# Optimization experiments

Measured on AMD Instinct MI355X. Metric: run time of the kernel, lower is better.

Reference implementation:

```python
import jax, jax.numpy as jnp
import numpy as np

NUM_HEADS = 16


def setup_inputs() -> dict:
    key = jax.random.key(0)
    ks = jax.random.split(key, 9)
    B, S, D = 2, 2048, 2048
    s = 1.0 / np.sqrt(D)
    return {
        "x": jax.random.normal(ks[0], (B, S, D), jnp.float32),
        "Wq": jax.random.normal(ks[1], (D, D), jnp.float32) * s,
        "bq": jax.random.normal(ks[2], (D,), jnp.float32) * 0.01,
        "Wk": jax.random.normal(ks[3], (D, D), jnp.float32) * s,
        "bk": jax.random.normal(ks[4], (D,), jnp.float32) * 0.01,
        "Wv": jax.random.normal(ks[5], (D, D), jnp.float32) * s,
        "bv": jax.random.normal(ks[6], (D,), jnp.float32) * 0.01,
        "Wo": jax.random.normal(ks[7], (D, D), jnp.float32) * s,
        "bo": jax.random.normal(ks[8], (D,), jnp.float32) * 0.01,
    }


def reference(x, Wq, bq, Wk, bk, Wv, bv, Wo, bo):
    B, S, D = x.shape
    H = NUM_HEADS
    dh = D // H
    # torch Linear: y = x @ W.T + b
    def proj(W, b):
        return (x @ W.T + b).reshape(B, S, H, dh).transpose(0, 2, 1, 3)  # [B,H,S,dh]
    Q = proj(Wq, bq)
    K = proj(Wk, bk)
    V = proj(Wv, bv)
    scores = jnp.einsum('bhqd,bhkd->bhqk', Q, K) / jnp.sqrt(jnp.float32(dh))
    causal = jnp.tril(jnp.ones((S, S), dtype=bool))  # allow k <= q
    scores = jnp.where(causal, scores, -jnp.inf)
    attn = jax.nn.softmax(scores, axis=-1)
    out = jnp.einsum('bhqk,bhkd->bhqd', attn, V)
    out = out.transpose(0, 2, 1, 3).reshape(B, S, D)
    return out @ Wo.T + bo
```

## Files before the change

### kernel.cpp

```cpp
#include <hip/hip_runtime.h>
#include <hip/hip_bf16.h>

#define B_  2
#define S_  2048
#define D_  2048
#define H_  16
#define DH_ 128
#define M_  (B_*S_)

typedef __hip_bfloat16 bf16;
typedef float v4f __attribute__((ext_vector_type(4)));
typedef short v8s __attribute__((ext_vector_type(8)));

__device__ __forceinline__ short f2s(float x) {
  bf16 h = __float2bfloat16(x);
  return *reinterpret_cast<const short*>(&h);
}
__device__ __forceinline__ v8s ld8(const float* p) {
  v4f a = *reinterpret_cast<const v4f*>(p);
  v4f b = *reinterpret_cast<const v4f*>(p + 4);
  v8s r = { f2s(a[0]), f2s(a[1]), f2s(a[2]), f2s(a[3]),
            f2s(b[0]), f2s(b[1]), f2s(b[2]), f2s(b[3]) };
  return r;
}
__device__ __forceinline__ void store_out(bf16* p, float v)  { *p = __float2bfloat16(v); }
__device__ __forceinline__ void store_out(float* p, float v) { *p = v; }

__device__ __forceinline__ void gll16(const bf16* g, bf16* l) {
  __builtin_amdgcn_global_load_lds((const __attribute__((address_space(1))) void*)g,
                                   (__attribute__((address_space(3))) void*)l,
                                   16, 0, 0);
}

__global__ __launch_bounds__(256) void cvt_f32_bf16(const float* __restrict__ in,
                                                    bf16* __restrict__ out, int n8) {
  int i = blockIdx.x * 256 + threadIdx.x;
  if (i >= n8) return;
  *reinterpret_cast<v8s*>(out + (size_t)i * 8) = ld8(in + (size_t)i * 8);
}

__global__ __launch_bounds__(256) void cvt3_f32_bf16(const float* __restrict__ a, bf16* __restrict__ oa,
                                                     const float* __restrict__ b, bf16* __restrict__ ob,
                                                     const float* __restrict__ c, bf16* __restrict__ oc) {
  const int bx = blockIdx.x;
  if (bx < 4096) {
    size_t i = (size_t)bx * 256 + threadIdx.x;
    *reinterpret_cast<v8s*>(oa + i * 8) = ld8(a + i * 8);
  } else if (bx < 6144) {
    size_t i = (size_t)(bx - 4096) * 256 + threadIdx.x;
    *reinterpret_cast<v8s*>(ob + i * 8) = ld8(b + i * 8);
  } else {
    size_t i = (size_t)(bx - 6144) * 256 + threadIdx.x;
    *reinterpret_cast<v8s*>(oc + i * 8) = ld8(c + i * 8);
  }
}

template <int MODE, typename TOUT>
__global__ __launch_bounds__(256) void gemm_bt(const bf16* __restrict__ A,
                                               const bf16* __restrict__ W,
                                               const float* __restrict__ bias0,
                                               const float* __restrict__ bias1,
                                               TOUT* __restrict__ out0,
                                               TOUT* __restrict__ out1) {
  __shared__ __align__(16) bf16 As[128 * 64];
  __shared__ __align__(16) bf16 Bs[128 * 64];
  const int tid  = threadIdx.x;
  const int lane = tid & 63, wave = tid >> 6;
  const int wm = wave >> 1, wn = wave & 1;
  const int quad = lane >> 4, l16 = lane & 15;
  const int swz  = l16 & 7;
  const int bm = blockIdx.y * 128, bn = blockIdx.x * 128;

  const bf16* Arow = A + (size_t)bm * D_;
  const bf16* Wrow = W + (size_t)bn * D_;

  v4f acc[4][4] = {};
  for (int k0 = 0; k0 < D_; k0 += 64) {
#pragma unroll
    for (int j = 0; j < 4; ++j) {
      const int blk = j * 256 + tid;
      const int row = blk >> 3, c = blk & 7;
      const int gcol = k0 + (((c ^ (row & 7)) << 3));
      gll16(Arow + (size_t)row * D_ + gcol, As + j * 2048 + wave * 512);
      gll16(Wrow + (size_t)row * D_ + gcol, Bs + j * 2048 + wave * 512);
    }
    __syncthreads();
    v8s af[4][2], bfr[4][2];
#pragma unroll
    for (int mi = 0; mi < 4; ++mi)
#pragma unroll
      for (int kk = 0; kk < 2; ++kk)
        af[mi][kk] = *reinterpret_cast<const v8s*>(
            &As[(wm * 64 + mi * 16 + l16) * 64 + (((kk * 4 + quad) ^ swz) << 3)]);
#pragma unroll
    for (int ni = 0; ni < 4; ++ni)
#pragma unroll
      for (int kk = 0; kk < 2; ++kk)
        bfr[ni][kk] = *reinterpret_cast<const v8s*>(
            &Bs[(wn * 64 + ni * 16 + l16) * 64 + (((kk * 4 + quad) ^ swz) << 3)]);
#pragma unroll
    for (int kk = 0; kk < 2; ++kk)
#pragma unroll
      for (int mi = 0; mi < 4; ++mi)
#pragma unroll
        for (int ni = 0; ni < 4; ++ni)
          acc[mi][ni] = __builtin_amdgcn_mfma_f32_16x16x32_bf16(
              af[mi][kk], bfr[ni][kk], acc[mi][ni], 0, 0, 0);
    __syncthreads();
  }

  constexpr float QSCALE = 0.12752003912f;
  const int proj = (MODE == 0) ? (bn >> 11) : 0;
  const float* bias = proj ? bias1 : bias0;
  TOUT* outp = proj ? out1 : out0;
  const int bnl = bn & 2047;
#pragma unroll
  for (int ni = 0; ni < 4; ++ni) {
    const int nl = bnl + wn * 64 + ni * 16 + l16;
    const float bv = bias[nl];
#pragma unroll
    for (int mi = 0; mi < 4; ++mi) {
      const int m0 = bm + wm * 64 + mi * 16 + quad * 4;
#pragma unroll
      for (int r = 0; r < 4; ++r) {
        const int m = m0 + r;
        float v = acc[mi][ni][r] + bv;
        size_t idx;
        if (MODE == 0) {
          if (!proj) v *= QSCALE;
          int b = m >> 11, s = m & (S_ - 1);
          int h = nl >> 7, d = nl & (DH_ - 1);
          idx = ((size_t)(b * H_ + h) * S_ + s) * DH_ + d;
        } else if (MODE == 2) {
          int b = m >> 11, s = m & (S_ - 1);
          int h = nl >> 7, d = nl & (DH_ - 1);
          idx = ((size_t)(b * H_ + h) * DH_ + d) * S_ + s;
        } else {
          idx = (size_t)m * D_ + nl;
        }
        store_out(outp + idx, v);
      }
    }
  }
}

#define QBLK 128
__global__ __launch_bounds__(512, 4) void attn_fused(const bf16* __restrict__ Q,
                                                     const bf16* __restrict__ K,
                                                     const bf16* __restrict__ Vt,
                                                     bf16* __restrict__ Oa) {
  __shared__ __align__(16) bf16 Ks[64 * 128];
  __shared__ __align__(16) bf16 Vs[128 * 64];
  __shared__ __align__(16) bf16 Ps[8][16 * 72];
  const int tid  = threadIdx.x;
  const int lane = tid & 63, wave = tid >> 6;
  const int quad = lane >> 4, l16 = lane & 15;
  const int swz  = l16 & 7;
  const int qtd = (int)gridDim.x - 1 - (int)blockIdx.x;
  const int qt  = (blockIdx.y & 16) ? (int)blockIdx.x : qtd;
  const int bh = blockIdx.y;
  const int b = bh >> 4, h = bh & 15;
  const bf16* Qh = Q  + (size_t)bh * S_ * DH_;
  const bf16* Kh = K  + (size_t)bh * S_ * DH_;
  const bf16* Vh = Vt + (size_t)bh * DH_ * S_;

  const int qrow0 = qt * QBLK + wave * 16;
  v8s qf[4];
#pragma unroll
  for (int kk = 0; kk < 4; ++kk)
    qf[kk] = *reinterpret_cast<const v8s*>(&Qh[(size_t)(qrow0 + l16) * DH_ + kk * 32 + quad * 8]);

  v4f acc_o[8] = {};
  float m_i[4], l_i[4];
#pragma unroll
  for (int r = 0; r < 4; ++r) { m_i[r] = -1.0e30f; l_i[r] = 0.f; }

  const int nkt = 2 * qt + 2;
  for (int kt = 0; kt < nkt; ++kt) {
    const int kbase = kt * 64;
#pragma unroll
    for (int rr = 0; rr < 2; ++rr) {
      const int g = rr * 512 + tid;
      const int krow = g >> 4, kc = g & 15;
      gll16(Kh + (size_t)(kbase + krow) * DH_ + ((kc ^ (krow & 7)) << 3),
            Ks + rr * 4096 + wave * 512);
      const int vrow = g >> 3, vc = g & 7;
      gll16(Vh + (size_t)vrow * S_ + kbase + ((vc ^ (vrow & 7)) << 3),
            Vs + rr * 4096 + wave * 512);
    }
    __syncthreads();

    const bool active = (kbase <= qrow0 + 15);
    if (active) {
      v4f sc[4];
      __builtin_amdgcn_s_setprio(1);
#pragma unroll
      for (int nt = 0; nt < 4; ++nt) {
        v4f a = {};
#pragma unroll
        for (int kk = 0; kk < 4; ++kk) {
          v8s kf = *reinterpret_cast<const v8s*>(
              &Ks[(nt * 16 + l16) * 128 + (((kk * 4 + quad) ^ swz) << 3)]);
          a = __builtin_amdgcn_mfma_f32_16x16x32_bf16(qf[kk], kf, a, 0, 0, 0);
        }
        sc[nt] = a;
      }
      __builtin_amdgcn_s_setprio(0);
      if (kbase + 63 > qrow0) {
#pragma unroll
        for (int nt = 0; nt < 4; ++nt)
#pragma unroll
          for (int r = 0; r < 4; ++r) {
            int kc2 = kbase + nt * 16 + l16;
            int qr = qrow0 + quad * 4 + r;
            if (kc2 > qr) sc[nt][r] = -1.0e30f;
          }
      }
#pragma unroll
      for (int r = 0; r < 4; ++r) {
        float mx = fmaxf(fmaxf(sc[0][r], sc[1][r]), fmaxf(sc[2][r], sc[3][r]));
        mx = fmaxf(mx, __shfl_xor(mx, 1));
        mx = fmaxf(mx, __shfl_xor(mx, 2));
        mx = fmaxf(mx, __shfl_xor(mx, 4));
        mx = fmaxf(mx, __shfl_xor(mx, 8));
        if (mx > m_i[r] + 8.0f) {
          float alpha = exp2f(m_i[r] - mx);
          m_i[r] = mx;
          l_i[r] *= alpha;
#pragma unroll
          for (int nt8 = 0; nt8 < 8; ++nt8) acc_o[nt8][r] *= alpha;
        }
        const float mm = m_i[r];
        float s0 = exp2f(sc[0][r] - mm);
        float s1 = exp2f(sc[1][r] - mm);
        float s2 = exp2f(sc[2][r] - mm);
        float s3 = exp2f(sc[3][r] - mm);
        sc[0][r] = s0; sc[1][r] = s1; sc[2][r] = s2; sc[3][r] = s3;
        float t = s0 + s1 + s2 + s3;
        t += __shfl_xor(t, 1); t += __shfl_xor(t, 2);
        t += __shfl_xor(t, 4); t += __shfl_xor(t, 8);
        l_i[r] += t;
      }
#pragma unroll
      for (int nt = 0; nt < 4; ++nt)
#pragma unroll
        for (int r = 0; r < 4; ++r)
          Ps[wave][(quad * 4 + r) * 72 + nt * 16 + l16] = __float2bfloat16(sc[nt][r]);
      asm volatile("s_waitcnt lgkmcnt(0)" ::: "memory");
      __builtin_amdgcn_s_setprio(1);
#pragma unroll
      for (int kk2 = 0; kk2 < 2; ++kk2) {
        v8s pf = *reinterpret_cast<const v8s*>(&Ps[wave][l16 * 72 + kk2 * 32 + quad * 8]);
#pragma unroll
        for (int nt8 = 0; nt8 < 8; ++nt8) {
          v8s vf = *reinterpret_cast<const v8s*>(
              &Vs[(nt8 * 16 + l16) * 64 + (((kk2 * 4 + quad) ^ swz) << 3)]);
          acc_o[nt8] = __builtin_amdgcn_mfma_f32_16x16x32_bf16(pf, vf, acc_o[nt8], 0, 0, 0);
        }
      }
      __builtin_amdgcn_s_setprio(0);
    }
    __syncthreads();
  }

#pragma unroll
  for (int r = 0; r < 4; ++r) {
    const float inv = 1.0f / l_i[r];
    const int srow = qrow0 + quad * 4 + r;
#pragma unroll
    for (int nt8 = 0; nt8 < 8; ++nt8)
      Oa[((size_t)b * S_ + srow) * D_ + h * DH_ + nt8 * 16 + l16] =
          __float2bfloat16(acc_o[nt8][r] * inv);
  }
}

extern "C" void kernel_launch(void* const* d_in, const int* in_sizes, int n_in,
                              void* d_out, int out_size, void* d_ws, size_t ws_size,
                              hipStream_t stream) {
  if (n_in != 9 ||
      in_sizes[0] != M_ * D_ ||
      in_sizes[1] != D_ * D_ || in_sizes[2] != D_ ||
      in_sizes[3] != D_ * D_ || in_sizes[4] != D_ ||
      in_sizes[5] != D_ * D_ || in_sizes[6] != D_ ||
      in_sizes[7] != D_ * D_ || in_sizes[8] != D_ ||
      out_size != M_ * D_)
    return;

  const float* x  = (const float*)d_in[0];
  const float* Wq = (const float*)d_in[1];
  const float* bq = (const float*)d_in[2];
  const float* Wk = (const float*)d_in[3];
  const float* bk = (const float*)d_in[4];
  const float* Wv = (const float*)d_in[5];
  const float* bv = (const float*)d_in[6];
  const float* Wo = (const float*)d_in[7];
  const float* bo = (const float*)d_in[8];
  float* out = (float*)d_out;

  const size_t NT = (size_t)M_ * D_;
  const size_t WN = (size_t)D_ * D_;
  bf16* qws   = (bf16*)d_out;
  bf16* xbf   = (bf16*)d_out + NT;
  bf16* kws   = (bf16*)d_ws;
  bf16* vtw   = kws + NT;
  bf16* aws   = vtw + NT;
  bf16* wqk   = aws;
  bf16* wv_s  = aws;
  bf16* wo_s  = kws;

  const int N8W = D_ * D_ / 8;

  dim3 bb(256);
  cvt3_f32_bf16<<<8192, bb, 0, stream>>>(x, xbf, Wq, wqk, Wk, wqk + WN);

  gemm_bt<0, bf16><<<dim3(32, 32), bb, 0, stream>>>(xbf, wqk, bq, bk, qws, kws);

  cvt_f32_bf16<<<N8W / 256, bb, 0, stream>>>(Wv, wv_s, N8W);
  gemm_bt<2, bf16><<<dim3(16, 32), bb, 0, stream>>>(xbf, wv_s, bv, bv, vtw, vtw);

  attn_fused<<<dim3(S_ / QBLK, B_ * H_), dim3(512), 0, stream>>>(qws, kws, vtw, aws);

  cvt_f32_bf16<<<N8W / 256, bb, 0, stream>>>(Wo, wo_s, N8W);
  gemm_bt<3, float><<<dim3(16, 32), bb, 0, stream>>>(aws, wo_s, bo, bo, out, out);
}
```

Baseline: 412.5 us.

## Add 256x256 double-buffered 8-wave GEMM for fused Q/K projection

Replaces the 128x128 single-buffered GEMM used for the combined Q/K projection with a 512-thread kernel that computes 256x256 tiles. Global-to-LDS loads for the next k-tile are issued in pieces interleaved with the MFMA phases, using ping-pong LDS buffers and explicit waitcnt/barriers. MFMA sections run at raised wave priority. The aim is more operand reuse per LDS load and hiding global load latency behind compute, at the cost of 128KB of LDS per block, fewer blocks (256), and fragile hand scheduling.

```diff
diff --git a/kernel.cpp b/kernel.cpp
--- a/kernel.cpp
+++ b/kernel.cpp
@@ -55,13 +55,156 @@
   }
 }
 
+template <int PR>
+__device__ __forceinline__ void stage_pair(const bf16* Arow, const bf16* Wrow,
+                                           int ktile, bf16* AsD, bf16* BsD,
+                                           int tid, int wave) {
+  const int k0 = ktile * 64;
+#pragma unroll
+  for (int u = 0; u < 2; ++u) {
+    const int i = PR * 2 + u;
+    const int blk = i * 512 + tid;
+    if (i < 4) {
+      const int row = blk >> 3, c = blk & 7;
+      gll16(Arow + (size_t)row * D_ + k0 + ((c ^ (row & 7)) << 3),
+            AsD + (i * 512 + wave * 64) * 8);
+    } else {
+      const int bb = blk - 2048;
+      const int row = bb >> 3, c = bb & 7;
+      gll16(Wrow + (size_t)row * D_ + k0 + ((c ^ (row & 7)) << 3),
+            BsD + ((i - 4) * 512 + wave * 64) * 8);
+    }
+  }
+}
+
+__global__ __launch_bounds__(512, 2) void gemm_qk8(const bf16* __restrict__ A,
+                                                   const bf16* __restrict__ W,
+                                                   const float* __restrict__ bias0,
+                                                   const float* __restrict__ bias1,
+                                                   bf16* __restrict__ out0,
+                                                   bf16* __restrict__ out1) {
+  __shared__ __align__(16) bf16 As0[256 * 64];
+  __shared__ __align__(16) bf16 Bs0[256 * 64];
+  __shared__ __align__(16) bf16 As1[256 * 64];
+  __shared__ __align__(16) bf16 Bs1[256 * 64];
+  const int tid  = threadIdx.x;
+  const int lane = tid & 63, wave = tid >> 6;
+  const int wm = wave >> 2, wn = wave & 3;
+  const int quad = lane >> 4, l16 = lane & 15;
+  const int swz  = l16 & 7;
+  const int bm = blockIdx.y * 256, bn = blockIdx.x * 256;
+  const bf16* Arow = A + (size_t)bm * D_;
+  const bf16* Wrow = W + (size_t)bn * D_;
+
+  v4f acc[8][4] = {};
+
+  stage_pair<0>(Arow, Wrow, 0, As0, Bs0, tid, wave);
+  stage_pair<1>(Arow, Wrow, 0, As0, Bs0, tid, wave);
+  stage_pair<2>(Arow, Wrow, 0, As0, Bs0, tid, wave);
+  stage_pair<3>(Arow, Wrow, 0, As0, Bs0, tid, wave);
+
+  constexpr int NITER = (D_ / 64) / 2;
+  for (int j = 0; j < NITER; ++j) {
+    const bool notlast = (j + 1 < NITER);
+#pragma unroll
+    for (int p = 0; p < 8; ++p) {
+      const bf16* Ard = (p < 4) ? As0 : As1;
+      const bf16* Brd = (p < 4) ? Bs0 : Bs1;
+      bf16* AsD = (p < 4) ? As1 : As0;
+      bf16* BsD = (p < 4) ? Bs1 : Bs0;
+      const int tstage = (p < 4) ? (2 * j + 1) : (2 * j + 2);
+
+      if (p == 0) {
+        stage_pair<0>(Arow, Wrow, tstage, AsD, BsD, tid, wave);
+        asm volatile("s_waitcnt vmcnt(2)" ::: "memory");
+        __builtin_amdgcn_sched_barrier(0);
+        __builtin_amdgcn_s_barrier();
+        __builtin_amdgcn_sched_barrier(0);
+      } else if (p == 4) {
+        if (notlast) {
+          stage_pair<0>(Arow, Wrow, tstage, AsD, BsD, tid, wave);
+          asm volatile("s_waitcnt vmcnt(2)" ::: "memory");
+        } else {
+          asm volatile("s_waitcnt vmcnt(0)" ::: "memory");
+        }
+        __builtin_amdgcn_sched_barrier(0);
+        __builtin_amdgcn_s_barrier();
+        __builtin_amdgcn_sched_barrier(0);
+      } else if (p < 4) {
+        if (p == 1) stage_pair<1>(Arow, Wrow, tstage, AsD, BsD, tid, wave);
+        if (p == 2) stage_pair<2>(Arow, Wrow, tstage, AsD, BsD, tid, wave);
+        if (p == 3) stage_pair<3>(Arow, Wrow, tstage, AsD, BsD, tid, wave);
+      } else {
+        if (notlast) {
+          if (p == 5) stage_pair<1>(Arow, Wrow, tstage, AsD, BsD, tid, wave);
+          if (p == 6) stage_pair<2>(Arow, Wrow, tstage, AsD, BsD, tid, wave);
+          if (p == 7) stage_pair<3>(Arow, Wrow, tstage, AsD, BsD, tid, wave);
+        }
+      }
+
+      const int pp = p & 3;
+      v8s af[2][2], bfr[4][2];
+#pragma unroll
+      for (int mi = 0; mi < 2; ++mi)
+#pragma unroll
+        for (int kk = 0; kk < 2; ++kk) {
+          const int row = wm * 128 + (pp * 2 + mi) * 16 + l16;
+          af[mi][kk] = *reinterpret_cast<const v8s*>(
+              &Ard[row * 64 + (((kk * 4 + quad) ^ swz) << 3)]);
+        }
+#pragma unroll
+      for (int ni = 0; ni < 4; ++ni)
+#pragma unroll
+        for (int kk = 0; kk < 2; ++kk) {
+          const int row = wn * 64 + ni * 16 + l16;
+          bfr[ni][kk] = *reinterpret_cast<const v8s*>(
+              &Brd[row * 64 + (((kk * 4 + quad) ^ swz) << 3)]);
+        }
+      __builtin_amdgcn_s_setprio(1);
+#pragma unroll
+      for (int kk = 0; kk < 2; ++kk)
+#pragma unroll
+        for (int mi = 0; mi < 2; ++mi)
+#pragma unroll
+          for (int ni = 0; ni < 4; ++ni)
+            acc[pp * 2 + mi][ni] = __builtin_amdgcn_mfma_f32_16x16x32_bf16(
+                af[mi][kk], bfr[ni][kk], acc[pp * 2 + mi][ni], 0, 0, 0);
+      __builtin_amdgcn_s_setprio(0);
+      __builtin_amdgcn_s_barrier();
+      __builtin_amdgcn_sched_barrier(0);
+    }
+  }
+
+  constexpr float QSCALE = 0.12752003912f;
+  const int proj = bn >> 11;
+  const float* bias = proj ? bias1 : bias0;
+  bf16* outp = proj ? out1 : out0;
+  const int bnl = bn & 2047;
+#pragma unroll
+  for (int ni = 0; ni < 4; ++ni) {
+    const int nl = bnl + wn * 64 + ni * 16 + l16;
+    const float bv = bias[nl];
+    const int hh = nl >> 7, d = nl & (DH_ - 1);
+#pragma unroll
+    for (int mi = 0; mi < 8; ++mi) {
+      const int m0 = bm + wm * 128 + mi * 16 + quad * 4;
+#pragma unroll
+      for (int r = 0; r < 4; ++r) {
+        const int m = m0 + r;
+        float v = acc[mi][ni][r] + bv;
+        if (!proj) v *= QSCALE;
+        const int bb = m >> 11, s = m & (S_ - 1);
+        outp[((size_t)(bb * H_ + hh) * S_ + s) * DH_ + d] = __float2bfloat16(v);
+      }
+    }
+  }
+}
+
 template <int MODE, typename TOUT>
 __global__ __launch_bounds__(256) void gemm_bt(const bf16* __restrict__ A,
                                                const bf16* __restrict__ W,
                                                const float* __restrict__ bias0,
-                                               const float* __restrict__ bias1,
-                                               TOUT* __restrict__ out0,
-                                               TOUT* __restrict__ out1) {
+                                               TOUT* __restrict__ out0) {
   __shared__ __align__(16) bf16 As[128 * 64];
   __shared__ __align__(16) bf16 Bs[128 * 64];
   const int tid  = threadIdx.x;
@@ -109,15 +252,10 @@
     __syncthreads();
   }
 
-  constexpr float QSCALE = 0.12752003912f;
-  const int proj = (MODE == 0) ? (bn >> 11) : 0;
-  const float* bias = proj ? bias1 : bias0;
-  TOUT* outp = proj ? out1 : out0;
-  const int bnl = bn & 2047;
 #pragma unroll
   for (int ni = 0; ni < 4; ++ni) {
-    const int nl = bnl + wn * 64 + ni * 16 + l16;
-    const float bv = bias[nl];
+    const int nl = bn + wn * 64 + ni * 16 + l16;
+    const float bv = bias0[nl];
 #pragma unroll
     for (int mi = 0; mi < 4; ++mi) {
       const int m0 = bm + wm * 64 + mi * 16 + quad * 4;
@@ -126,19 +264,14 @@
         const int m = m0 + r;
         float v = acc[mi][ni][r] + bv;
         size_t idx;
-        if (MODE == 0) {
-          if (!proj) v *= QSCALE;
-          int b = m >> 11, s = m & (S_ - 1);
-          int h = nl >> 7, d = nl & (DH_ - 1);
-          idx = ((size_t)(b * H_ + h) * S_ + s) * DH_ + d;
-        } else if (MODE == 2) {
+        if (MODE == 2) {
           int b = m >> 11, s = m & (S_ - 1);
           int h = nl >> 7, d = nl & (DH_ - 1);
           idx = ((size_t)(b * H_ + h) * DH_ + d) * S_ + s;
         } else {
           idx = (size_t)m * D_ + nl;
         }
-        store_out(outp + idx, v);
+        store_out(out0 + idx, v);
       }
     }
   }
@@ -313,13 +446,13 @@
   dim3 bb(256);
   cvt3_f32_bf16<<<8192, bb, 0, stream>>>(x, xbf, Wq, wqk, Wk, wqk + WN);
 
-  gemm_bt<0, bf16><<<dim3(32, 32), bb, 0, stream>>>(xbf, wqk, bq, bk, qws, kws);
+  gemm_qk8<<<dim3(16, 16), dim3(512), 0, stream>>>(xbf, wqk, bq, bk, qws, kws);
 
   cvt_f32_bf16<<<N8W / 256, bb, 0, stream>>>(Wv, wv_s, N8W);
-  gemm_bt<2, bf16><<<dim3(16, 32), bb, 0, stream>>>(xbf, wv_s, bv, bv, vtw, vtw);
+  gemm_bt<2, bf16><<<dim3(16, 32), bb, 0, stream>>>(xbf, wv_s, bv, vtw);
 
   attn_fused<<<dim3(S_ / QBLK, B_ * H_), dim3(512), 0, stream>>>(qws, kws, vtw, aws);
 
   cvt_f32_bf16<<<N8W / 256, bb, 0, stream>>>(Wo, wo_s, N8W);
-  gemm_bt<3, float><<<dim3(16, 32), bb, 0, stream>>>(aws, wo_s, bo, bo, out, out);
-}
+  gemm_bt<3, float><<<dim3(16, 32), bb, 0, stream>>>(aws, wo_s, bo, out);
+}
```

Result: no change. 407.1 us (-1.3%).
